# Kernel tuning notes

Measured on AMD Instinct MI355X. Metric: run time of the kernel, lower is better.

## Reference

```python
import jax, jax.numpy as jnp
import numpy as np
import math

INPUT_SIZE = 512
DK = 64
B, N = 8, 2048

def setup_inputs() -> dict:
    key = jax.random.key(0)
    k1, k2, k3, k4, k5, k6 = jax.random.split(key, 6)
    X = jax.random.normal(k1, (B, N, INPUT_SIZE), dtype=jnp.float32)
    h = jax.random.normal(k2, (B, N, INPUT_SIZE), dtype=jnp.float32)
    s = 1.0 / math.sqrt(INPUT_SIZE)
    WQ = jax.random.uniform(k3, (INPUT_SIZE, DK), dtype=jnp.float32, minval=-s, maxval=s)
    bQ = jax.random.uniform(k4, (DK,), dtype=jnp.float32, minval=-s, maxval=s)
    WK = jax.random.uniform(k5, (INPUT_SIZE, DK), dtype=jnp.float32, minval=-s, maxval=s)
    bK = jax.random.uniform(k6, (DK,), dtype=jnp.float32, minval=-s, maxval=s)
    return {"X": X, "h": h, "WQ": WQ, "bQ": bQ, "WK": WK, "bK": bK}

def reference(X, h, WQ, bQ, WK, bK):
    # Q = linearQ(h), K = linearK(X); dropout is eval-mode identity
    Q = jnp.einsum('bnd,dk->bnk', h, WQ) + bQ   # [B, N, dk]
    K = jnp.einsum('bnd,dk->bnk', X, WK) + bK   # [B, N, dk]
    scores = jnp.einsum('bqk,bnk->bqn', Q, K) / jnp.sqrt(jnp.asarray(DK, X.dtype))
    A = jax.nn.softmax(scores, axis=-1)          # [B, N, N]
    out = jnp.einsum('bqn,bnd->bqd', A, X)       # V = X
    return out
```

## Files before the change

### kernel.cpp

```cpp
#include <hip/hip_runtime.h>
#include <hip/hip_bf16.h>

#define B_ 8
#define N_ 2048
#define D_ 512
#define DK_ 64

typedef float f32x4 __attribute__((ext_vector_type(4)));
typedef short bf16x8 __attribute__((ext_vector_type(8)));
typedef unsigned short u16;

__device__ __forceinline__ u16 f2bf(float f) {
  union { float f; unsigned u; } v; v.f = f;
  unsigned r = v.u + 0x7FFFu + ((v.u >> 16) & 1u);
  return (u16)(r >> 16);
}

#define MFMA32(a, b, cacc) __builtin_amdgcn_mfma_f32_16x16x32_bf16((a), (b), (cacc), 0, 0, 0)

#define BARRIER_LGKM() do {                                   \
    asm volatile("s_waitcnt lgkmcnt(0)" ::: "memory");        \
    __builtin_amdgcn_s_barrier();                             \
    asm volatile("" ::: "memory");                            \
  } while (0)


__global__ __launch_bounds__(256) void prep_kernel(
    const float* __restrict__ h, const float* __restrict__ X,
    const float* __restrict__ WQ, const float* __restrict__ bQ,
    const float* __restrict__ WK, const float* __restrict__ bK,
    u16* __restrict__ Qf, u16* __restrict__ Kf, u16* __restrict__ Vf) {
  int bid = blockIdx.x;
  int b = bid & 7, nt = bid >> 3;
  int n0 = nt * 64;
  int t = threadIdx.x, w = t >> 6, l = t & 63, g = l >> 4, c = l & 15;

  __shared__ u16 Xb16[64][520];

  int arow = n0 + w * 16 + c;
  const float* hrow = h + ((size_t)b * N_ + arow) * D_;
  const float* Xrow = X + ((size_t)b * N_ + arow) * D_;
  f32x4 accq[4], acck[4];
#pragma unroll
  for (int cf = 0; cf < 4; ++cf) {
    accq[cf] = (f32x4){0.f, 0.f, 0.f, 0.f};
    acck[cf] = (f32x4){0.f, 0.f, 0.f, 0.f};
  }
  for (int k0 = 0; k0 < D_; k0 += 32) {
    bf16x8 ah, ax;
    {
      f32x4 h0 = *reinterpret_cast<const f32x4*>(hrow + k0 + 8 * g);
      f32x4 h1 = *reinterpret_cast<const f32x4*>(hrow + k0 + 8 * g + 4);
      f32x4 x0 = *reinterpret_cast<const f32x4*>(Xrow + k0 + 8 * g);
      f32x4 x1 = *reinterpret_cast<const f32x4*>(Xrow + k0 + 8 * g + 4);
#pragma unroll
      for (int i = 0; i < 4; ++i) {
        ah[i] = (short)f2bf(h0[i]); ah[i + 4] = (short)f2bf(h1[i]);
        ax[i] = (short)f2bf(x0[i]); ax[i + 4] = (short)f2bf(x1[i]);
      }
    }
    *reinterpret_cast<bf16x8*>(&Xb16[w * 16 + c][k0 + 8 * g]) = ax;
#pragma unroll
    for (int cf = 0; cf < 4; ++cf) {
      bf16x8 bq, bk;
#pragma unroll
      for (int i = 0; i < 8; ++i) {
        int kk = k0 + 8 * g + i;
        bq[i] = (short)f2bf(WQ[(size_t)kk * DK_ + cf * 16 + c]);
        bk[i] = (short)f2bf(WK[(size_t)kk * DK_ + cf * 16 + c]);
      }
      accq[cf] = MFMA32(ah, bq, accq[cf]);
      acck[cf] = MFMA32(ax, bk, acck[cf]);
    }
  }
#pragma unroll
  for (int cf = 0; cf < 4; ++cf) {
    float vq = bQ[cf * 16 + c], vk = bK[cf * 16 + c];
    int ks = cf >> 1;
    int g2 = ((cf & 1) * 16 + c) >> 3;
    int i2 = c & 7;
#pragma unroll
    for (int r = 0; r < 4; ++r) {
      size_t e = ((size_t)(b * 128 + nt * 4 + w) * 2 + ks) * 512 +
                 (g2 * 16 + 4 * g + r) * 8 + i2;
      Qf[e] = f2bf((accq[cf][r] + vq) * 0.125f);
      Kf[e] = f2bf(acck[cf][r] + vk);
    }
  }

  __syncthreads();

#pragma unroll
  for (int dtl = 0; dtl < 8; ++dtl) {
    int dt = w * 8 + dtl;
#pragma unroll
    for (int ks = 0; ks < 2; ++ks) {
      bf16x8 v;
#pragma unroll
      for (int i = 0; i < 8; ++i) v[i] = Xb16[ks * 32 + 8 * g + i][dt * 16 + c];
      *reinterpret_cast<bf16x8*>(
          Vf + (((size_t)(b * 32 + dt) * 32 + nt) * 2 + ks) * 512 + l * 8) = v;
    }
  }
}

__global__ __launch_bounds__(1024, 4) void attn_kernel(
    const u16* __restrict__ Qf, const u16* __restrict__ Kf,
    const u16* __restrict__ Vf, float* __restrict__ out) {
  int bid = blockIdx.x;
  int b = bid & 7, qt = bid >> 3;
  int q0 = qt * 64;
  int t = threadIdx.x, w = t >> 6, l = t & 63, g = l >> 4, c = l & 15;
  int qh = (w >> 1) & 3, kq = w & 1;
  const bool prod = (w < 8);

  __shared__ u16 Plds[4][64][40];
  __shared__ float Lp[2][64];

  bf16x8 aq[2];
  if (prod) {
#pragma unroll
    for (int ks = 0; ks < 2; ++ks)
      aq[ks] = *reinterpret_cast<const bf16x8*>(
          Qf + ((size_t)(b * 128 + qt * 4 + qh) * 2 + ks) * 512 + l * 8);
  }

  f32x4 o[4][2];
#pragma unroll
  for (int a = 0; a < 4; ++a)
#pragma unroll
    for (int f = 0; f < 2; ++f) o[a][f] = (f32x4){0.f, 0.f, 0.f, 0.f};
  float lp[4] = {0.f, 0.f, 0.f, 0.f};

  const u16* Kbase = Kf + ((size_t)(b * 256 + 2 * kq)) * 512 + l * 8;
  const u16* Vbase = Vf + ((size_t)(b * 32 + w * 2) * 64) * 512 + l * 8;

  bf16x8 kb0[2], kb1[2], vb0[2], vb1[2];

  if (prod) {
#pragma unroll
    for (int ks = 0; ks < 2; ++ks) {
      kb0[ks] = *reinterpret_cast<const bf16x8*>(Kbase + (size_t)ks * 512);
      kb1[ks] = *reinterpret_cast<const bf16x8*>(Kbase + (size_t)(4 + ks) * 512);
    }
  }
#pragma unroll
  for (int f = 0; f < 2; ++f) {
    vb0[f] = *reinterpret_cast<const bf16x8*>(Vbase + (size_t)(f * 64 + 0) * 512);
    vb1[f] = *reinterpret_cast<const bf16x8*>(Vbase + (size_t)(f * 64 + 1) * 512);
  }
  if (prod) {
    {
      f32x4 s = (f32x4){0.f, 0.f, 0.f, 0.f};
      s = MFMA32(aq[0], kb0[0], s); s = MFMA32(aq[1], kb0[1], s);
#pragma unroll
      for (int r = 0; r < 4; ++r) {
        float p = __expf(s[r]); lp[r] += p;
        Plds[0][qh * 16 + 4 * g + r][kq * 16 + c] = f2bf(p);
      }
    }
    {
      f32x4 s = (f32x4){0.f, 0.f, 0.f, 0.f};
      s = MFMA32(aq[0], kb1[0], s); s = MFMA32(aq[1], kb1[1], s);
#pragma unroll
      for (int r = 0; r < 4; ++r) {
        float p = __expf(s[r]); lp[r] += p;
        Plds[1][qh * 16 + 4 * g + r][kq * 16 + c] = f2bf(p);
      }
    }
  }
  BARRIER_LGKM();

  auto pair = [&](int k2, int pR0, int pR1, int pW0, int pW1) {
    if (prod) {
#pragma unroll
      for (int ks = 0; ks < 2; ++ks) {
        kb0[ks] = *reinterpret_cast<const bf16x8*>(
            Kbase + (size_t)(4 * (k2 + 2) + ks) * 512);
        kb1[ks] = *reinterpret_cast<const bf16x8*>(
            Kbase + (size_t)(4 * (k2 + 3) + ks) * 512);
      }
    }

    {
      bf16x8 pa0 = *reinterpret_cast<const bf16x8*>(&Plds[pR0][c][8 * g]);
      bf16x8 pa1 = *reinterpret_cast<const bf16x8*>(&Plds[pR0][16 + c][8 * g]);
      bf16x8 pa2 = *reinterpret_cast<const bf16x8*>(&Plds[pR0][32 + c][8 * g]);
      bf16x8 pa3 = *reinterpret_cast<const bf16x8*>(&Plds[pR0][48 + c][8 * g]);
      __builtin_amdgcn_s_setprio(1);
#pragma unroll
      for (int f = 0; f < 2; ++f) {
        o[0][f] = MFMA32(pa0, vb0[f], o[0][f]);
        o[1][f] = MFMA32(pa1, vb0[f], o[1][f]);
        o[2][f] = MFMA32(pa2, vb0[f], o[2][f]);
        o[3][f] = MFMA32(pa3, vb0[f], o[3][f]);
      }
      __builtin_amdgcn_s_setprio(0);
    }
#pragma unroll
    for (int f = 0; f < 2; ++f)
      vb0[f] = *reinterpret_cast<const bf16x8*>(
          Vbase + (size_t)(f * 64 + k2 + 2) * 512);

    {
      bf16x8 pa0 = *reinterpret_cast<const bf16x8*>(&Plds[pR1][c][8 * g]);
      bf16x8 pa1 = *reinterpret_cast<const bf16x8*>(&Plds[pR1][16 + c][8 * g]);
      bf16x8 pa2 = *reinterpret_cast<const bf16x8*>(&Plds[pR1][32 + c][8 * g]);
      bf16x8 pa3 = *reinterpret_cast<const bf16x8*>(&Plds[pR1][48 + c][8 * g]);
      __builtin_amdgcn_s_setprio(1);
#pragma unroll
      for (int f = 0; f < 2; ++f) {
        o[0][f] = MFMA32(pa0, vb1[f], o[0][f]);
        o[1][f] = MFMA32(pa1, vb1[f], o[1][f]);
        o[2][f] = MFMA32(pa2, vb1[f], o[2][f]);
        o[3][f] = MFMA32(pa3, vb1[f], o[3][f]);
      }
      __builtin_amdgcn_s_setprio(0);
    }
#pragma unroll
    for (int f = 0; f < 2; ++f)
      vb1[f] = *reinterpret_cast<const bf16x8*>(
          Vbase + (size_t)(f * 64 + k2 + 3) * 512);

    if (prod) {
      {
        f32x4 s = (f32x4){0.f, 0.f, 0.f, 0.f};
        s = MFMA32(aq[0], kb0[0], s); s = MFMA32(aq[1], kb0[1], s);
#pragma unroll
        for (int r = 0; r < 4; ++r) {
          float p = __expf(s[r]); lp[r] += p;
          Plds[pW0][qh * 16 + 4 * g + r][kq * 16 + c] = f2bf(p);
        }
      }
      {
        f32x4 s = (f32x4){0.f, 0.f, 0.f, 0.f};
        s = MFMA32(aq[0], kb1[0], s); s = MFMA32(aq[1], kb1[1], s);
#pragma unroll
        for (int r = 0; r < 4; ++r) {
          float p = __expf(s[r]); lp[r] += p;
          Plds[pW1][qh * 16 + 4 * g + r][kq * 16 + c] = f2bf(p);
        }
      }
    }

    BARRIER_LGKM();
  };

#pragma unroll 1
  for (int k2 = 0; k2 < 60; k2 += 4) {
    pair(k2, 0, 1, 2, 3);
    pair(k2 + 2, 2, 3, 0, 1);
  }
  pair(60, 0, 1, 2, 3);

#pragma unroll
  for (int e = 0; e < 2; ++e) {
    const int pb = 2 + e;
    bf16x8 pa0 = *reinterpret_cast<const bf16x8*>(&Plds[pb][c][8 * g]);
    bf16x8 pa1 = *reinterpret_cast<const bf16x8*>(&Plds[pb][16 + c][8 * g]);
    bf16x8 pa2 = *reinterpret_cast<const bf16x8*>(&Plds[pb][32 + c][8 * g]);
    bf16x8 pa3 = *reinterpret_cast<const bf16x8*>(&Plds[pb][48 + c][8 * g]);
#pragma unroll
    for (int f = 0; f < 2; ++f) {
      bf16x8 vv = e ? vb1[f] : vb0[f];
      o[0][f] = MFMA32(pa0, vv, o[0][f]);
      o[1][f] = MFMA32(pa1, vv, o[1][f]);
      o[2][f] = MFMA32(pa2, vv, o[2][f]);
      o[3][f] = MFMA32(pa3, vv, o[3][f]);
    }
  }

  if (prod) {
#pragma unroll
    for (int r = 0; r < 4; ++r) {
      float v = lp[r];
      v += __shfl_xor(v, 1); v += __shfl_xor(v, 2);
      v += __shfl_xor(v, 4); v += __shfl_xor(v, 8);
      lp[r] = v;
    }
    if (c == 0) {
#pragma unroll
      for (int r = 0; r < 4; ++r) Lp[kq][qh * 16 + 4 * g + r] = lp[r];
    }
  }
  __syncthreads();

  float* outb = out + ((size_t)b * N_ + q0) * D_;
#pragma unroll
  for (int a = 0; a < 4; ++a)
#pragma unroll
    for (int r = 0; r < 4; ++r) {
      int ql = a * 16 + 4 * g + r;
      float L = Lp[0][ql] + Lp[1][ql];
      float inv = 1.0f / L;
#pragma unroll
      for (int f = 0; f < 2; ++f)
        outb[(size_t)ql * D_ + w * 32 + f * 16 + c] = o[a][f][r] * inv;
    }
}

extern "C" void kernel_launch(void* const* d_in, const int* in_sizes, int n_in,
                              void* d_out, int out_size, void* d_ws, size_t ws_size,
                              hipStream_t stream) {
  const float* X  = (const float*)d_in[0];
  const float* h  = (const float*)d_in[1];
  const float* WQ = (const float*)d_in[2];
  const float* bQ = (const float*)d_in[3];
  const float* WK = (const float*)d_in[4];
  const float* bK = (const float*)d_in[5];
  float* out = (float*)d_out;

  u16* Vf = (u16*)d_ws;
  u16* Qf = Vf + (size_t)B_ * D_ * N_;
  u16* Kf = Qf + (size_t)B_ * N_ * DK_;

  prep_kernel<<<dim3(256), dim3(256), 0, stream>>>(h, X, WQ, bQ, WK, bK, Qf, Kf, Vf);
  attn_kernel<<<dim3(256), dim3(1024), 0, stream>>>(Qf, Kf, Vf, out);
}
```

Measured before the change: 74.71 us.

## Retile attention blocks to 128 queries by half head dimension with 8 waves

Each block now handles 128 query rows and half of the 512-wide value dimension using 8 waves, instead of 64 query rows over the full dimension with 16 waves. Every wave now computes scores and exponentials for two query sub-tiles and accumulates 8x2 output tiles, so V fragments are reused across twice as many query rows. The split between producer and consumer waves is removed. Scores and exponentials are now computed redundantly by both dimension-half blocks, and register pressure per wave rises.

```diff
diff --git a/kernel.cpp b/kernel.cpp
--- a/kernel.cpp
+++ b/kernel.cpp
@@ -104,144 +104,107 @@
   }
 }
 
-__global__ __launch_bounds__(1024, 4) void attn_kernel(
+__global__ __launch_bounds__(512, 1) void attn_kernel(
     const u16* __restrict__ Qf, const u16* __restrict__ Kf,
     const u16* __restrict__ Vf, float* __restrict__ out) {
   int bid = blockIdx.x;
-  int b = bid & 7, qt = bid >> 3;
-  int q0 = qt * 64;
+  int b = bid & 7, dh = (bid >> 3) & 1, qt = bid >> 4;
+  int q0 = qt * 128;
   int t = threadIdx.x, w = t >> 6, l = t & 63, g = l >> 4, c = l & 15;
-  int qh = (w >> 1) & 3, kq = w & 1;
-  const bool prod = (w < 8);
-
-  __shared__ u16 Plds[4][64][40];
-  __shared__ float Lp[2][64];
-
-  bf16x8 aq[2];
-  if (prod) {
-#pragma unroll
-    for (int ks = 0; ks < 2; ++ks)
-      aq[ks] = *reinterpret_cast<const bf16x8*>(
-          Qf + ((size_t)(b * 128 + qt * 4 + qh) * 2 + ks) * 512 + l * 8);
-  }
-
-  f32x4 o[4][2];
-#pragma unroll
-  for (int a = 0; a < 4; ++a)
+  int kq = w & 1, qhA = w >> 1, qhB = 4 + (w >> 1);
+
+  __shared__ u16 Plds[4][128][40];
+  __shared__ float Lp[2][128];
+
+  bf16x8 aqA[2], aqB[2];
+#pragma unroll
+  for (int ks = 0; ks < 2; ++ks) {
+    aqA[ks] = *reinterpret_cast<const bf16x8*>(
+        Qf + ((size_t)(b * 128 + qt * 8 + qhA) * 2 + ks) * 512 + l * 8);
+    aqB[ks] = *reinterpret_cast<const bf16x8*>(
+        Qf + ((size_t)(b * 128 + qt * 8 + qhB) * 2 + ks) * 512 + l * 8);
+  }
+
+  f32x4 o[8][2];
+#pragma unroll
+  for (int a = 0; a < 8; ++a)
 #pragma unroll
     for (int f = 0; f < 2; ++f) o[a][f] = (f32x4){0.f, 0.f, 0.f, 0.f};
-  float lp[4] = {0.f, 0.f, 0.f, 0.f};
+  float lpA[4] = {0.f, 0.f, 0.f, 0.f}, lpB[4] = {0.f, 0.f, 0.f, 0.f};
 
   const u16* Kbase = Kf + ((size_t)(b * 256 + 2 * kq)) * 512 + l * 8;
-  const u16* Vbase = Vf + ((size_t)(b * 32 + w * 2) * 64) * 512 + l * 8;
+  const u16* Vbase = Vf + ((size_t)(b * 32 + dh * 16 + w * 2) * 64) * 512 + l * 8;
 
   bf16x8 kb0[2], kb1[2], vb0[2], vb1[2];
 
-  if (prod) {
-#pragma unroll
-    for (int ks = 0; ks < 2; ++ks) {
-      kb0[ks] = *reinterpret_cast<const bf16x8*>(Kbase + (size_t)ks * 512);
-      kb1[ks] = *reinterpret_cast<const bf16x8*>(Kbase + (size_t)(4 + ks) * 512);
-    }
+  auto sexp = [&](bf16x8 (&kb)[2], int pb) {
+    {
+      f32x4 s = (f32x4){0.f, 0.f, 0.f, 0.f};
+      s = MFMA32(aqA[0], kb[0], s); s = MFMA32(aqA[1], kb[1], s);
+#pragma unroll
+      for (int r = 0; r < 4; ++r) {
+        float p = __expf(s[r]); lpA[r] += p;
+        Plds[pb][qhA * 16 + 4 * g + r][kq * 16 + c] = f2bf(p);
+      }
+    }
+    {
+      f32x4 s = (f32x4){0.f, 0.f, 0.f, 0.f};
+      s = MFMA32(aqB[0], kb[0], s); s = MFMA32(aqB[1], kb[1], s);
+#pragma unroll
+      for (int r = 0; r < 4; ++r) {
+        float p = __expf(s[r]); lpB[r] += p;
+        Plds[pb][qhB * 16 + 4 * g + r][kq * 16 + c] = f2bf(p);
+      }
+    }
+  };
+  auto pv = [&](int pb, bf16x8 (&vb)[2]) {
+    __builtin_amdgcn_s_setprio(1);
+#pragma unroll
+    for (int a = 0; a < 8; ++a) {
+      bf16x8 pa = *reinterpret_cast<const bf16x8*>(&Plds[pb][a * 16 + c][8 * g]);
+      o[a][0] = MFMA32(pa, vb[0], o[a][0]);
+      o[a][1] = MFMA32(pa, vb[1], o[a][1]);
+    }
+    __builtin_amdgcn_s_setprio(0);
+  };
+
+#pragma unroll
+  for (int ks = 0; ks < 2; ++ks) {
+    kb0[ks] = *reinterpret_cast<const bf16x8*>(Kbase + (size_t)ks * 512);
+    kb1[ks] = *reinterpret_cast<const bf16x8*>(Kbase + (size_t)(4 + ks) * 512);
   }
 #pragma unroll
   for (int f = 0; f < 2; ++f) {
     vb0[f] = *reinterpret_cast<const bf16x8*>(Vbase + (size_t)(f * 64 + 0) * 512);
     vb1[f] = *reinterpret_cast<const bf16x8*>(Vbase + (size_t)(f * 64 + 1) * 512);
   }
-  if (prod) {
-    {
-      f32x4 s = (f32x4){0.f, 0.f, 0.f, 0.f};
-      s = MFMA32(aq[0], kb0[0], s); s = MFMA32(aq[1], kb0[1], s);
-#pragma unroll
-      for (int r = 0; r < 4; ++r) {
-        float p = __expf(s[r]); lp[r] += p;
-        Plds[0][qh * 16 + 4 * g + r][kq * 16 + c] = f2bf(p);
-      }
-    }
-    {
-      f32x4 s = (f32x4){0.f, 0.f, 0.f, 0.f};
-      s = MFMA32(aq[0], kb1[0], s); s = MFMA32(aq[1], kb1[1], s);
-#pragma unroll
-      for (int r = 0; r < 4; ++r) {
-        float p = __expf(s[r]); lp[r] += p;
-        Plds[1][qh * 16 + 4 * g + r][kq * 16 + c] = f2bf(p);
-      }
-    }
-  }
+  sexp(kb0, 0);
+  sexp(kb1, 1);
   BARRIER_LGKM();
 
   auto pair = [&](int k2, int pR0, int pR1, int pW0, int pW1) {
-    if (prod) {
-#pragma unroll
-      for (int ks = 0; ks < 2; ++ks) {
-        kb0[ks] = *reinterpret_cast<const bf16x8*>(
-            Kbase + (size_t)(4 * (k2 + 2) + ks) * 512);
-        kb1[ks] = *reinterpret_cast<const bf16x8*>(
-            Kbase + (size_t)(4 * (k2 + 3) + ks) * 512);
-      }
-    }
-
-    {
-      bf16x8 pa0 = *reinterpret_cast<const bf16x8*>(&Plds[pR0][c][8 * g]);
-      bf16x8 pa1 = *reinterpret_cast<const bf16x8*>(&Plds[pR0][16 + c][8 * g]);
-      bf16x8 pa2 = *reinterpret_cast<const bf16x8*>(&Plds[pR0][32 + c][8 * g]);
-      bf16x8 pa3 = *reinterpret_cast<const bf16x8*>(&Plds[pR0][48 + c][8 * g]);
-      __builtin_amdgcn_s_setprio(1);
-#pragma unroll
-      for (int f = 0; f < 2; ++f) {
-        o[0][f] = MFMA32(pa0, vb0[f], o[0][f]);
-        o[1][f] = MFMA32(pa1, vb0[f], o[1][f]);
-        o[2][f] = MFMA32(pa2, vb0[f], o[2][f]);
-        o[3][f] = MFMA32(pa3, vb0[f], o[3][f]);
-      }
-      __builtin_amdgcn_s_setprio(0);
-    }
+#pragma unroll
+    for (int ks = 0; ks < 2; ++ks) {
+      kb0[ks] = *reinterpret_cast<const bf16x8*>(
+          Kbase + (size_t)(4 * (k2 + 2) + ks) * 512);
+      kb1[ks] = *reinterpret_cast<const bf16x8*>(
+          Kbase + (size_t)(4 * (k2 + 3) + ks) * 512);
+    }
+
+    pv(pR0, vb0);
 #pragma unroll
     for (int f = 0; f < 2; ++f)
       vb0[f] = *reinterpret_cast<const bf16x8*>(
           Vbase + (size_t)(f * 64 + k2 + 2) * 512);
 
-    {
-      bf16x8 pa0 = *reinterpret_cast<const bf16x8*>(&Plds[pR1][c][8 * g]);
-      bf16x8 pa1 = *reinterpret_cast<const bf16x8*>(&Plds[pR1][16 + c][8 * g]);
-      bf16x8 pa2 = *reinterpret_cast<const bf16x8*>(&Plds[pR1][32 + c][8 * g]);
-      bf16x8 pa3 = *reinterpret_cast<const bf16x8*>(&Plds[pR1][48 + c][8 * g]);
-      __builtin_amdgcn_s_setprio(1);
-#pragma unroll
-      for (int f = 0; f < 2; ++f) {
-        o[0][f] = MFMA32(pa0, vb1[f], o[0][f]);
-        o[1][f] = MFMA32(pa1, vb1[f], o[1][f]);
-        o[2][f] = MFMA32(pa2, vb1[f], o[2][f]);
-        o[3][f] = MFMA32(pa3, vb1[f], o[3][f]);
-      }
-      __builtin_amdgcn_s_setprio(0);
-    }
+    pv(pR1, vb1);
 #pragma unroll
     for (int f = 0; f < 2; ++f)
       vb1[f] = *reinterpret_cast<const bf16x8*>(
           Vbase + (size_t)(f * 64 + k2 + 3) * 512);
 
-    if (prod) {
-      {
-        f32x4 s = (f32x4){0.f, 0.f, 0.f, 0.f};
-        s = MFMA32(aq[0], kb0[0], s); s = MFMA32(aq[1], kb0[1], s);
-#pragma unroll
-        for (int r = 0; r < 4; ++r) {
-          float p = __expf(s[r]); lp[r] += p;
-          Plds[pW0][qh * 16 + 4 * g + r][kq * 16 + c] = f2bf(p);
-        }
-      }
-      {
-        f32x4 s = (f32x4){0.f, 0.f, 0.f, 0.f};
-        s = MFMA32(aq[0], kb1[0], s); s = MFMA32(aq[1], kb1[1], s);
-#pragma unroll
-        for (int r = 0; r < 4; ++r) {
-          float p = __expf(s[r]); lp[r] += p;
-          Plds[pW1][qh * 16 + 4 * g + r][kq * 16 + c] = f2bf(p);
-        }
-      }
-    }
+    sexp(kb0, pW0);
+    sexp(kb1, pW1);
 
     BARRIER_LGKM();
   };
@@ -253,41 +216,30 @@
   }
   pair(60, 0, 1, 2, 3);
 
-#pragma unroll
-  for (int e = 0; e < 2; ++e) {
-    const int pb = 2 + e;
-    bf16x8 pa0 = *reinterpret_cast<const bf16x8*>(&Plds[pb][c][8 * g]);
-    bf16x8 pa1 = *reinterpret_cast<const bf16x8*>(&Plds[pb][16 + c][8 * g]);
-    bf16x8 pa2 = *reinterpret_cast<const bf16x8*>(&Plds[pb][32 + c][8 * g]);
-    bf16x8 pa3 = *reinterpret_cast<const bf16x8*>(&Plds[pb][48 + c][8 * g]);
-#pragma unroll
-    for (int f = 0; f < 2; ++f) {
-      bf16x8 vv = e ? vb1[f] : vb0[f];
-      o[0][f] = MFMA32(pa0, vv, o[0][f]);
-      o[1][f] = MFMA32(pa1, vv, o[1][f]);
-      o[2][f] = MFMA32(pa2, vv, o[2][f]);
-      o[3][f] = MFMA32(pa3, vv, o[3][f]);
-    }
-  }
-
-  if (prod) {
+  pv(2, vb0);
+  pv(3, vb1);
+
+#pragma unroll
+  for (int r = 0; r < 4; ++r) {
+    float vA = lpA[r], vB = lpB[r];
+    vA += __shfl_xor(vA, 1); vA += __shfl_xor(vA, 2);
+    vA += __shfl_xor(vA, 4); vA += __shfl_xor(vA, 8);
+    vB += __shfl_xor(vB, 1); vB += __shfl_xor(vB, 2);
+    vB += __shfl_xor(vB, 4); vB += __shfl_xor(vB, 8);
+    lpA[r] = vA; lpB[r] = vB;
+  }
+  if (c == 0) {
 #pragma unroll
     for (int r = 0; r < 4; ++r) {
-      float v = lp[r];
-      v += __shfl_xor(v, 1); v += __shfl_xor(v, 2);
-      v += __shfl_xor(v, 4); v += __shfl_xor(v, 8);
-      lp[r] = v;
-    }
-    if (c == 0) {
-#pragma unroll
-      for (int r = 0; r < 4; ++r) Lp[kq][qh * 16 + 4 * g + r] = lp[r];
+      Lp[kq][qhA * 16 + 4 * g + r] = lpA[r];
+      Lp[kq][qhB * 16 + 4 * g + r] = lpB[r];
     }
   }
   __syncthreads();
 
-  float* outb = out + ((size_t)b * N_ + q0) * D_;
-#pragma unroll
-  for (int a = 0; a < 4; ++a)
+  float* outb = out + ((size_t)b * N_ + q0) * D_ + dh * 256;
+#pragma unroll
+  for (int a = 0; a < 8; ++a)
 #pragma unroll
     for (int r = 0; r < 4; ++r) {
       int ql = a * 16 + 4 * g + r;
@@ -315,5 +267,5 @@
   u16* Kf = Qf + (size_t)B_ * N_ * DK_;
 
   prep_kernel<<<dim3(256), dim3(256), 0, stream>>>(h, X, WQ, bQ, WK, bK, Qf, Kf, Vf);
-  attn_kernel<<<dim3(256), dim3(1024), 0, stream>>>(Qf, Kf, Vf, out);
-}
+  attn_kernel<<<dim3(256), dim3(512), 0, stream>>>(Qf, Kf, Vf, out);
+}
```

Measured after the change: 80.81 us. 8.2% more time.
